# Kernel tuning notes

Hardware: AMD Instinct MI355X
Metric: run time of the kernel (lower is better)

## Reference

```python
import jax, jax.numpy as jnp
import numpy as np
import math

N_H = 16
REL_K = 16  # relative-position clamp window


def setup_inputs() -> dict:
    key = jax.random.key(0)
    ks = jax.random.split(key, 7)
    B, S, D = 8, 1024, 1024
    d_k = D // N_H
    scale = 0.02
    return {
        "x": jax.random.normal(ks[0], (B, S, D), dtype=jnp.float32),
        "W_attn": jax.random.normal(ks[1], (D, 3 * D), dtype=jnp.float32) * scale,
        "b_attn": jax.random.normal(ks[2], (3 * D,), dtype=jnp.float32) * scale,
        "W_proj": jax.random.normal(ks[3], (D, D), dtype=jnp.float32) * scale,
        "b_proj": jax.random.normal(ks[4], (D,), dtype=jnp.float32) * scale,
        "lut_k": jax.random.normal(ks[5], (2 * REL_K + 1, d_k), dtype=jnp.float32) * scale,
        "lut_v": jax.random.normal(ks[6], (2 * REL_K + 1, d_k), dtype=jnp.float32) * scale,
    }


def reference(x, W_attn, b_attn, W_proj, b_proj, lut_k, lut_v):
    B, S, D = x.shape
    d_k = D // N_H

    qkv = x @ W_attn + b_attn  # [B, S, 3D]
    q, k, v = jnp.split(qkv, 3, axis=-1)
    # [B, H, S, d_k]
    q = q.reshape(B, S, N_H, d_k).transpose(0, 2, 1, 3)
    k = k.reshape(B, S, N_H, d_k).transpose(0, 2, 1, 3)
    v = v.reshape(B, S, N_H, d_k).transpose(0, 2, 1, 3)

    i = jnp.arange(S)[:, None]
    j = jnp.arange(S)[None, :]
    rel = jnp.clip(j - i, -REL_K, REL_K) + REL_K  # [S, S] in [0, 2k]
    aij_k = lut_k[rel]  # [S, S, d_k]
    aij_v = lut_v[rel]  # [S, S, d_k]

    scores = jnp.einsum('bhid,bhjd->bhij', q, k)
    scores = scores + jnp.einsum('bhid,ijd->bhij', q, aij_k)
    scores = scores * (1.0 / math.sqrt(d_k))

    causal = j <= i  # [S, S]
    scores = jnp.where(causal[None, None, :, :], scores, -jnp.inf)
    attn = jax.nn.softmax(scores, axis=-1)  # [B, H, S, S]

    out = jnp.einsum('bhij,bhjd->bhid', attn, v)
    out = out + jnp.einsum('bhij,ijd->bhid', attn, aij_v)
    out = out.transpose(0, 2, 1, 3).reshape(B, S, D)
    return out @ W_proj + b_proj
```

## Files before the change

kernel.cpp:

```cpp
#include <hip/hip_runtime.h>
#include <hip/hip_bf16.h>
#include <math.h>

#define NH 16
#define S_LEN 1024
#define DK 64
#define D_MODEL 1024
#define HSZ 8388608

typedef __attribute__((ext_vector_type(8))) short bf16x8;
typedef __attribute__((ext_vector_type(4))) float f32x4;
typedef unsigned short USH;

#define EXPSCALE 0.1803368801111204f

__device__ __forceinline__ float fast_exp2(float x) {
    return __builtin_amdgcn_exp2f(x);
}

__device__ __forceinline__ short f2b(float x) {
    union { __hip_bfloat16 h; short s; } u;
    u.h = __float2bfloat16(x);
    return u.s;
}
__device__ __forceinline__ float b2f(USH u) {
    union { unsigned i; float f; } x;
    x.i = (unsigned)u << 16;
    return x.f;
}

__device__ __forceinline__ void gload16(const void* src, void* lds) {
    __builtin_amdgcn_global_load_lds(
        (const __attribute__((address_space(1))) void*)src,
        (__attribute__((address_space(3))) void*)lds,
        16, 0, 0);
}

__global__ __launch_bounds__(256)
void conv_bf16_kernel(const float* __restrict__ in, USH* __restrict__ out) {
    const int i = (blockIdx.x * 256 + threadIdx.x) * 8;
    const float4 a = *(const float4*)&in[i];
    const float4 b = *(const float4*)&in[i + 4];
    ushort4 o0, o1;
    o0.x = (USH)f2b(a.x); o0.y = (USH)f2b(a.y); o0.z = (USH)f2b(a.z); o0.w = (USH)f2b(a.w);
    o1.x = (USH)f2b(b.x); o1.y = (USH)f2b(b.y); o1.z = (USH)f2b(b.z); o1.w = (USH)f2b(b.w);
    *(ushort4*)&out[i] = o0;
    *(ushort4*)&out[i + 4] = o1;
}

__global__ __launch_bounds__(256)
void transp_bf16_kernel(const float* __restrict__ in, USH* __restrict__ out,
                        int R, int C) {
    __shared__ USH Ts[64][65];
    const int r0 = blockIdx.y * 64, c0 = blockIdx.x * 64;
    const int tr = threadIdx.x >> 4;
    const int tc4 = (threadIdx.x & 15) * 4;
    #pragma unroll
    for (int ph = 0; ph < 4; ++ph) {
        const int r = ph * 16 + tr;
        const float4 v = *(const float4*)&in[(size_t)(r0 + r) * C + c0 + tc4];
        Ts[tc4 + 0][r] = (USH)f2b(v.x);
        Ts[tc4 + 1][r] = (USH)f2b(v.y);
        Ts[tc4 + 2][r] = (USH)f2b(v.z);
        Ts[tc4 + 3][r] = (USH)f2b(v.w);
    }
    __syncthreads();
    #pragma unroll
    for (int ph = 0; ph < 4; ++ph) {
        const int cc = ph * 16 + tr;
        ushort4 o;
        o.x = Ts[cc][tc4 + 0]; o.y = Ts[cc][tc4 + 1];
        o.z = Ts[cc][tc4 + 2]; o.w = Ts[cc][tc4 + 3];
        *(ushort4*)&out[(size_t)(c0 + cc) * R + r0 + tc4] = o;
    }
}

__global__ __launch_bounds__(256)
void vtransp_kernel(const USH* __restrict__ in, USH* __restrict__ out) {
    __shared__ USH T[64][72];
    const int bh = blockIdx.x >> 4;
    const int s0 = (blockIdx.x & 15) * 64;
    const int r = threadIdx.x >> 4;
    const int c4 = (threadIdx.x & 15) * 4;
    #pragma unroll
    for (int ph = 0; ph < 4; ++ph) {
        const int row = ph * 16 + r;
        const ushort4 v = *(const ushort4*)
            &in[((size_t)bh * S_LEN + s0 + row) * DK + c4];
        T[row][c4 + 0] = v.x; T[row][c4 + 1] = v.y;
        T[row][c4 + 2] = v.z; T[row][c4 + 3] = v.w;
    }
    __syncthreads();
    #pragma unroll
    for (int ph = 0; ph < 4; ++ph) {
        const int d = ph * 16 + r;
        ushort4 o;
        o.x = T[c4 + 0][d]; o.y = T[c4 + 1][d];
        o.z = T[c4 + 2][d]; o.w = T[c4 + 3][d];
        *(ushort4*)&out[(size_t)bh * (S_LEN * DK) + (size_t)d * S_LEN + s0 + c4] = o;
    }
}

template<int QKV>
__global__ __launch_bounds__(256)
void mfma_gemm_kernel(const USH* __restrict__ A, const USH* __restrict__ Bt,
                      const float* __restrict__ bias,
                      float* __restrict__ Cf, USH* __restrict__ Cq,
                      USH* __restrict__ Ck, USH* __restrict__ Cv,
                      int M, int N, int K) {
    __shared__ __align__(16) USH As[128 * 32];
    __shared__ __align__(16) USH Bs[128 * 32];
    const int t = threadIdx.x;
    const int w = t >> 6, lane = t & 63, g = lane >> 4, c = lane & 15;
    const int wm = w >> 1, wn = w & 1;
    const int bm0 = blockIdx.y * 128, bn0 = blockIdx.x * 128;

    const int sk = ((t & 3) ^ ((t >> 3) & 3)) * 8;
    const USH* pa0 = A + (size_t)(bm0 + (t >> 2)) * K + sk;
    const USH* pa1 = pa0 + (size_t)64 * K;
    const USH* pb0 = Bt + (size_t)(bn0 + (t >> 2)) * K + sk;
    const USH* pb1 = pb0 + (size_t)64 * K;
    USH* ldsA0 = &As[(t & ~63) * 8];
    USH* ldsA1 = ldsA0 + 2048;
    USH* ldsB0 = &Bs[(t & ~63) * 8];
    USH* ldsB1 = ldsB0 + 2048;

    unsigned aoff[4], boff[4];
    #pragma unroll
    for (int i = 0; i < 4; ++i) {
        const int r = wm * 64 + i * 16 + c;
        aoff[i] = ((unsigned)(r * 64 + g * 16)) ^ ((((unsigned)r >> 1) & 3) << 4);
        const int n = wn * 64 + i * 16 + c;
        boff[i] = ((unsigned)(n * 64 + g * 16)) ^ ((((unsigned)n >> 1) & 3) << 4);
    }

    f32x4 acc[4][4];
    #pragma unroll
    for (int i = 0; i < 4; ++i)
        #pragma unroll
        for (int j = 0; j < 4; ++j) acc[i][j] = (f32x4)0.f;

    for (int k0 = 0; k0 < K; k0 += 32) {
        gload16(pa0 + k0, ldsA0);
        gload16(pa1 + k0, ldsA1);
        gload16(pb0 + k0, ldsB0);
        gload16(pb1 + k0, ldsB1);
        __syncthreads();

        bf16x8 af[4], bfr[4];
        #pragma unroll
        for (int i = 0; i < 4; ++i) af[i] = *(const bf16x8*)((const char*)As + aoff[i]);
        #pragma unroll
        for (int j = 0; j < 4; ++j) bfr[j] = *(const bf16x8*)((const char*)Bs + boff[j]);
        #pragma unroll
        for (int i = 0; i < 4; ++i)
            #pragma unroll
            for (int j = 0; j < 4; ++j)
                acc[i][j] = __builtin_amdgcn_mfma_f32_16x16x32_bf16(
                    af[i], bfr[j], acc[i][j], 0, 0, 0);
        __syncthreads();
    }

    #pragma unroll
    for (int i = 0; i < 4; ++i) {
        #pragma unroll
        for (int reg = 0; reg < 4; ++reg) {
            const int m = bm0 + wm * 64 + i * 16 + g * 4 + reg;
            #pragma unroll
            for (int j = 0; j < 4; ++j) {
                const int n = bn0 + wn * 64 + j * 16 + c;
                const float v = acc[i][j][reg] + bias[n];
                if (QKV) {
                    const int which = n >> 10;
                    const int h = (n & 1023) >> 6, d = n & 63;
                    const int b = m >> 10, s = m & 1023;
                    const size_t idx = (((size_t)(b * NH + h)) * S_LEN + s) * DK + d;
                    if (which == 0)      Cq[idx] = (USH)f2b(v);
                    else if (which == 1) Ck[idx] = (USH)f2b(v);
                    else                 Cv[idx] = (USH)f2b(v);
                } else {
                    Cf[(size_t)m * N + n] = v;
                }
            }
        }
    }
}

__global__ __launch_bounds__(512, 4)
void attn_mfma_kernel(const USH* __restrict__ qb,
                      const USH* __restrict__ kbuf,
                      const USH* __restrict__ vtg,
                      const float* __restrict__ lut_k,
                      const float* __restrict__ lut_v,
                      USH* __restrict__ ao) {
    const int bid = blockIdx.x;
    const int logical = (bid & 7) * 128 + (bid >> 3);
    const int ib = 7 - (logical & 7);
    const int bh = logical >> 3;
    const int b = bh >> 4, h = bh & 15;
    const int i0 = ib * 128;
    const int t = threadIdx.x;
    const int w = t >> 6;
    const int lane = t & 63;
    const int g = lane >> 4;
    const int c = lane & 15;

    __shared__ __align__(16) char smem[76928];
    char* pb     = smem + 49152;
    char* qsb    = smem + 49152;
    char* lutkb  = smem + 8192;
    USH* qrelb   = (USH*)(smem + 65536);
    USH* lvfb    = (USH*)(smem + 70656);
    USH* tapssb  = (USH*)(smem + 72832);

    const USH* qp  = qb   + (size_t)bh * (S_LEN * DK);
    const USH* kp  = kbuf + (size_t)bh * (S_LEN * DK);
    const USH* vtp = vtg  + (size_t)bh * (S_LEN * DK);

    auto stage = [&](int j0, int slot) {
        const int o = t * 16;
        const int row = o >> 7;
        const int chunk = (o >> 4) & 7;
        const int sc = (chunk ^ (row & 7)) * 8;
        gload16(kp + (size_t)(j0 + row) * DK + sc, smem + slot * 8192 + o);
        gload16(vtp + (size_t)row * S_LEN + j0 + sc, smem + 24576 + slot * 8192 + o);
    };

    stage(0, 0);
    for (int f = t; f < 2048; f += 512) {
        const int row = f >> 4, c4 = (f & 15) * 4;
        unsigned byte = ((unsigned)(row * 128 + c4 * 2)) ^ (((unsigned)row & 7) << 4);
        *(ushort4*)(qsb + byte) = *(const ushort4*)&qp[(size_t)(i0 + row) * DK + c4];
    }
    for (int e = t; e < 32 * 64; e += 512) {
        const int row = e >> 6, d = e & 63;
        const USH v = (row < 17) ? (USH)f2b(lut_k[row * 64 + d]) : (USH)0;
        unsigned byte = ((unsigned)(row * 128 + d * 2)) ^ (((unsigned)row & 7) << 4);
        *(USH*)(lutkb + byte) = v;
    }
    for (int e = t; e < 17 * 64; e += 512)
        lvfb[e] = (USH)f2b(lut_v[e]);
    __syncthreads();

    bf16x8 qa[2];
    {
        const int row = w * 16 + c;
        #pragma unroll
        for (int kh = 0; kh < 2; ++kh) {
            unsigned byte = ((unsigned)(row * 128 + kh * 64 + g * 16))
                          ^ (((unsigned)row & 7) << 4);
            qa[kh] = *(const bf16x8*)(qsb + byte);
        }
    }

    {
        f32x4 qr[2];
        qr[0] = (f32x4)0.f; qr[1] = (f32x4)0.f;
        #pragma unroll
        for (int sub2 = 0; sub2 < 2; ++sub2) {
            const int tap = sub2 * 16 + c;
            #pragma unroll
            for (int kh = 0; kh < 2; ++kh) {
                unsigned byte = ((unsigned)(tap * 128 + kh * 64 + g * 16))
                              ^ (((unsigned)tap & 7) << 4);
                bf16x8 lb = *(const bf16x8*)(lutkb + byte);
                qr[sub2] = __builtin_amdgcn_mfma_f32_16x16x32_bf16(
                    qa[kh], lb, qr[sub2], 0, 0, 0);
            }
        }
        #pragma unroll
        for (int sub2 = 0; sub2 < 2; ++sub2) {
            const int tap = sub2 * 16 + c;
            if (tap < 17) {
                #pragma unroll
                for (int r = 0; r < 4; ++r)
                    qrelb[(w * 16 + g * 4 + r) * 20 + tap] = (USH)f2b(qr[sub2][r]);
            }
        }
    }
    float qrel0s[4];
    #pragma unroll
    for (int r = 0; r < 4; ++r)
        qrel0s[r] = b2f(qrelb[(w * 16 + g * 4 + r) * 20]) * EXPSCALE;

    __syncthreads();

    const int NT = 2 * ib + 2;
    if (1 < NT) stage(64, 1);

    f32x4 acc[4];
    #pragma unroll
    for (int dt = 0; dt < 4; ++dt) acc[dt] = (f32x4)0.f;
    float l_r[4];
    #pragma unroll
    for (int r = 0; r < 4; ++r) l_r[r] = 0.f;

    const int wrow0 = i0 + w * 16;
    int cur = 0;
    for (int tile = 0; tile < NT; ++tile) {
        const int nxt2 = tile + 2;
        const int slot2 = (cur + 2 >= 3) ? cur - 1 : cur + 2;
        if (nxt2 < NT)
            stage(nxt2 << 6, slot2);

        if (tile * 64 > wrow0 + 15) {
            if (nxt2 < NT) asm volatile("s_waitcnt vmcnt(2)" ::: "memory");
            else           asm volatile("s_waitcnt vmcnt(0)" ::: "memory");
            __builtin_amdgcn_s_barrier();
            cur = (cur + 1 == 3) ? 0 : cur + 1;
            continue;
        }

        const char* ktb = smem + cur * 8192;
        const char* vtb = smem + 24576 + cur * 8192;

        float p[4][4];
        __builtin_amdgcn_s_setprio(1);
        f32x4 s[4];
        #pragma unroll
        for (int sub = 0; sub < 4; ++sub) {
            s[sub] = (f32x4)0.f;
            const int krow = sub * 16 + c;
            #pragma unroll
            for (int kh = 0; kh < 2; ++kh) {
                unsigned byte = ((unsigned)krow << 7) + ((unsigned)kh << 6) + ((unsigned)g << 4);
                byte ^= (unsigned)(krow & 7) << 4;
                bf16x8 kb = *(const bf16x8*)(ktb + byte);
                s[sub] = __builtin_amdgcn_mfma_f32_16x16x32_bf16(qa[kh], kb, s[sub], 0, 0, 0);
            }
        }
        __builtin_amdgcn_s_setprio(0);

        if (tile * 64 + 79 <= wrow0) {
            #pragma unroll
            for (int sub = 0; sub < 4; ++sub)
                #pragma unroll
                for (int r = 0; r < 4; ++r)
                    p[sub][r] = fast_exp2(s[sub][r] * EXPSCALE + qrel0s[r]);
        } else {
            #pragma unroll
            for (int sub = 0; sub < 4; ++sub) {
                const int dbase = tile * 64 + (sub * 16 + c) - i0 - (w * 16 + g * 4);
                #pragma unroll
                for (int r = 0; r < 4; ++r) {
                    const int dj = dbase - r;
                    int t17 = dj + 16;
                    t17 = t17 < 0 ? 0 : (t17 > 16 ? 16 : t17);
                    const int il = w * 16 + g * 4 + r;
                    float pv = fast_exp2((s[sub][r] + b2f(qrelb[il * 20 + t17])) * EXPSCALE);
                    if (dj > 0) pv = 0.f;
                    p[sub][r] = pv;
                    if (dj >= -15 && dj <= 0)
                        tapssb[il * 16 + dj + 15] = (USH)f2b(pv);
                }
            }
        }

        #pragma unroll
        for (int r = 0; r < 4; ++r)
            l_r[r] += (p[0][r] + p[1][r]) + (p[2][r] + p[3][r]);

        char* pw = pb + w * 2048;
        #pragma unroll
        for (int sub = 0; sub < 4; ++sub)
            #pragma unroll
            for (int r = 0; r < 4; ++r) {
                const int row = g * 4 + r;
                unsigned byte = ((unsigned)row << 7) + (((unsigned)(sub * 16 + c)) << 1);
                byte ^= (unsigned)(row & 7) << 4;
                *(short*)(pw + byte) = f2b(p[sub][r]);
            }

        bf16x8 pa[2];
        #pragma unroll
        for (int jh = 0; jh < 2; ++jh) {
            unsigned byte = ((unsigned)c << 7) + ((unsigned)jh << 6) + ((unsigned)g << 4);
            byte ^= (unsigned)(c & 7) << 4;
            pa[jh] = *(const bf16x8*)(pw + byte);
        }
        __builtin_amdgcn_s_setprio(1);
        #pragma unroll
        for (int dt = 0; dt < 4; ++dt) {
            const int d = dt * 16 + c;
            #pragma unroll
            for (int jh = 0; jh < 2; ++jh) {
                unsigned byte = ((unsigned)d << 7) + ((unsigned)jh << 6) + ((unsigned)g << 4);
                byte ^= (unsigned)(d & 7) << 4;
                bf16x8 vb = *(const bf16x8*)(vtb + byte);
                acc[dt] = __builtin_amdgcn_mfma_f32_16x16x32_bf16(pa[jh], vb, acc[dt], 0, 0, 0);
            }
        }
        __builtin_amdgcn_s_setprio(0);

        if (nxt2 < NT) asm volatile("s_waitcnt vmcnt(2)" ::: "memory");
        else           asm volatile("s_waitcnt vmcnt(0)" ::: "memory");
        __builtin_amdgcn_s_barrier();
        cur = (cur + 1 == 3) ? 0 : cur + 1;
    }

    const int rbase = w * 16 + g * 4;
    #pragma unroll
    for (int r = 0; r < 4; ++r) {
        float lsum = l_r[r];
        #pragma unroll
        for (int msk = 1; msk < 16; msk <<= 1)
            lsum += __shfl_xor(lsum, msk);
        const int il = rbase + r;
        float c0 = lsum;
        float tp[16];
        #pragma unroll
        for (int tap = 0; tap < 16; ++tap) {
            const int jg = i0 + il + tap - 15;
            const float pv = (jg >= 0) ? b2f(tapssb[il * 16 + tap]) : 0.f;
            tp[tap] = pv;
            c0 -= pv;
        }
        const float invl = 1.f / lsum;
        #pragma unroll
        for (int dt = 0; dt < 4; ++dt) {
            const int d = dt * 16 + c;
            float o = acc[dt][r] + c0 * b2f(lvfb[d]);
            #pragma unroll
            for (int tap = 0; tap < 16; ++tap)
                o += tp[tap] * b2f(lvfb[(tap + 1) * 64 + d]);
            o *= invl;
            ao[((size_t)b * S_LEN + (i0 + il)) * D_MODEL + h * DK + d] = (USH)f2b(o);
        }
    }
}

extern "C" void kernel_launch(void* const* d_in, const int* in_sizes, int n_in,
                              void* d_out, int out_size, void* d_ws, size_t ws_size,
                              hipStream_t stream) {
    const float* x      = (const float*)d_in[0];
    const float* W_attn = (const float*)d_in[1];
    const float* b_attn = (const float*)d_in[2];
    const float* W_proj = (const float*)d_in[3];
    const float* b_proj = (const float*)d_in[4];
    const float* lut_k  = (const float*)d_in[5];
    const float* lut_v  = (const float*)d_in[6];
    float* out = (float*)d_out;

    USH* qb    = (USH*)d_ws;
    USH* kb    = qb + HSZ;
    USH* vb    = kb + HSZ;
    USH* vtg   = vb + HSZ;
    USH* aob   = vtg + HSZ;
    USH* xb    = aob + HSZ;
    USH* watt  = xb + HSZ;
    USH* wproj = watt + 3145728;

    conv_bf16_kernel<<<HSZ / (256 * 8), 256, 0, stream>>>(x, xb);
    transp_bf16_kernel<<<dim3(3072 / 64, 1024 / 64), 256, 0, stream>>>(
        W_attn, watt, 1024, 3072);
    transp_bf16_kernel<<<dim3(1024 / 64, 1024 / 64), 256, 0, stream>>>(
        W_proj, wproj, 1024, 1024);

    mfma_gemm_kernel<1><<<dim3(3072 / 128, 8192 / 128), 256, 0, stream>>>(
        xb, watt, b_attn, nullptr, qb, kb, vb, 8192, 3072, 1024);

    vtransp_kernel<<<2048, 256, 0, stream>>>(vb, vtg);

    attn_mfma_kernel<<<1024, 512, 0, stream>>>(qb, kb, vtg, lut_k, lut_v, aob);

    mfma_gemm_kernel<0><<<dim3(1024 / 128, 8192 / 128), 256, 0, stream>>>(
        aob, wproj, b_proj, out, nullptr, nullptr, nullptr, 8192, 1024, 1024);
}
```

Baseline: 208.0 us.

## Merge prep kernels and rewrite QKV GEMM with 256x256 tiles and triple-buffered LDS

Merges the x conversion and both weight transposes into one prep kernel to save launches. Replaces the QKV GEMM with a 512-thread kernel using 256x256 output tiles and a three-slot LDS ring filled by direct global-to-LDS loads with vmcnt waits, plus s_setprio around the MFMAs and a swizzled block order for L2 reuse. This aims to increase data reuse per LDS byte and overlap global loads with MFMA work. It uses 96KB of LDS and a large accumulator set, which may limit occupancy.

Measured after the change: 199.2 us. -4.2%, faster.

```diff
diff --git a/kernel.cpp b/kernel.cpp
--- a/kernel.cpp
+++ b/kernel.cpp
@@ -37,24 +37,37 @@
 }
 
 __global__ __launch_bounds__(256)
-void conv_bf16_kernel(const float* __restrict__ in, USH* __restrict__ out) {
-    const int i = (blockIdx.x * 256 + threadIdx.x) * 8;
-    const float4 a = *(const float4*)&in[i];
-    const float4 b = *(const float4*)&in[i + 4];
-    ushort4 o0, o1;
-    o0.x = (USH)f2b(a.x); o0.y = (USH)f2b(a.y); o0.z = (USH)f2b(a.z); o0.w = (USH)f2b(a.w);
-    o1.x = (USH)f2b(b.x); o1.y = (USH)f2b(b.y); o1.z = (USH)f2b(b.z); o1.w = (USH)f2b(b.w);
-    *(ushort4*)&out[i] = o0;
-    *(ushort4*)&out[i + 4] = o1;
-}
-
-__global__ __launch_bounds__(256)
-void transp_bf16_kernel(const float* __restrict__ in, USH* __restrict__ out,
-                        int R, int C) {
+void prep_kernel(const float* __restrict__ x, USH* __restrict__ xb,
+                 const float* __restrict__ W_attn, USH* __restrict__ watt,
+                 const float* __restrict__ W_proj, USH* __restrict__ wproj) {
+    const int blk = blockIdx.x;
+    const int t = threadIdx.x;
+    if (blk < 4096) {
+        const int i = (blk * 256 + t) * 8;
+        const float4 a = *(const float4*)&x[i];
+        const float4 b = *(const float4*)&x[i + 4];
+        ushort4 o0, o1;
+        o0.x = (USH)f2b(a.x); o0.y = (USH)f2b(a.y); o0.z = (USH)f2b(a.z); o0.w = (USH)f2b(a.w);
+        o1.x = (USH)f2b(b.x); o1.y = (USH)f2b(b.y); o1.z = (USH)f2b(b.z); o1.w = (USH)f2b(b.w);
+        *(ushort4*)&xb[i] = o0;
+        *(ushort4*)&xb[i + 4] = o1;
+        return;
+    }
     __shared__ USH Ts[64][65];
-    const int r0 = blockIdx.y * 64, c0 = blockIdx.x * 64;
-    const int tr = threadIdx.x >> 4;
-    const int tc4 = (threadIdx.x & 15) * 4;
+    const float* in;
+    USH* out;
+    int R, C, r0, c0;
+    if (blk < 4864) {
+        const int idx = blk - 4096;
+        in = W_attn; out = watt; R = 1024; C = 3072;
+        c0 = (idx % 48) * 64; r0 = (idx / 48) * 64;
+    } else {
+        const int idx = blk - 4864;
+        in = W_proj; out = wproj; R = 1024; C = 1024;
+        c0 = (idx % 16) * 64; r0 = (idx / 16) * 64;
+    }
+    const int tr = t >> 4;
+    const int tc4 = (t & 15) * 4;
     #pragma unroll
     for (int ph = 0; ph < 4; ++ph) {
         const int r = ph * 16 + tr;
@@ -101,12 +114,109 @@
     }
 }
 
-template<int QKV>
+__global__ __launch_bounds__(512)
+void qkv_gemm_kernel(const USH* __restrict__ A, const USH* __restrict__ Bt,
+                     const float* __restrict__ bias,
+                     USH* __restrict__ Cq, USH* __restrict__ Ck,
+                     USH* __restrict__ Cv) {
+    __shared__ __align__(16) USH lds[3 * 16384];
+    const int t = threadIdx.x;
+    const int w = t >> 6, lane = t & 63, g = lane >> 4, c = lane & 15;
+    const int wm = w >> 2, wn = w & 3;
+    const int bid = blockIdx.x;
+    const int swz = (bid & 7) * 48 + (bid >> 3);
+    const int bn0 = (swz % 12) * 256;
+    const int bm0 = (swz / 12) * 256;
+
+    auto stage = [&](int kt, int slot) {
+        const int k0 = kt * 32;
+        USH* base = lds + slot * 16384;
+        #pragma unroll
+        for (int q = 0; q < 2; ++q) {
+            const int o = t * 16 + q * 8192;
+            const int row = o >> 6;
+            const int chunk = (o >> 4) & 3;
+            const int sc = (chunk ^ (row & 3)) * 8;
+            gload16(A + (size_t)(bm0 + row) * 1024 + k0 + sc, (char*)base + o);
+            gload16(Bt + (size_t)(bn0 + row) * 1024 + k0 + sc,
+                    (char*)(base + 8192) + o);
+        }
+    };
+
+    unsigned aoff[8], boff[4];
+    #pragma unroll
+    for (int i = 0; i < 8; ++i) {
+        const int row = wm * 128 + i * 16 + c;
+        aoff[i] = (unsigned)(row * 64) + (((unsigned)(g ^ (row & 3))) << 4);
+    }
+    #pragma unroll
+    for (int j = 0; j < 4; ++j) {
+        const int row = wn * 64 + j * 16 + c;
+        boff[j] = 16384u + (unsigned)(row * 64) + (((unsigned)(g ^ (row & 3))) << 4);
+    }
+
+    f32x4 acc[8][4];
+    #pragma unroll
+    for (int i = 0; i < 8; ++i)
+        #pragma unroll
+        for (int j = 0; j < 4; ++j) acc[i][j] = (f32x4)0.f;
+
+    stage(0, 0);
+    stage(1, 1);
+
+    int cur = 0;
+    for (int kt = 0; kt < 32; ++kt) {
+        if (kt < 31) asm volatile("s_waitcnt vmcnt(4)" ::: "memory");
+        else         asm volatile("s_waitcnt vmcnt(0)" ::: "memory");
+        __builtin_amdgcn_s_barrier();
+
+        const int slot2 = (cur + 2 >= 3) ? cur - 1 : cur + 2;
+        if (kt + 2 < 32)
+            stage(kt + 2, slot2);
+
+        const char* sb = (const char*)lds + cur * 32768;
+        bf16x8 af[8], bfr[4];
+        #pragma unroll
+        for (int i = 0; i < 8; ++i) af[i] = *(const bf16x8*)(sb + aoff[i]);
+        #pragma unroll
+        for (int j = 0; j < 4; ++j) bfr[j] = *(const bf16x8*)(sb + boff[j]);
+
+        __builtin_amdgcn_s_setprio(1);
+        #pragma unroll
+        for (int i = 0; i < 8; ++i)
+            #pragma unroll
+            for (int j = 0; j < 4; ++j)
+                acc[i][j] = __builtin_amdgcn_mfma_f32_16x16x32_bf16(
+                    af[i], bfr[j], acc[i][j], 0, 0, 0);
+        __builtin_amdgcn_s_setprio(0);
+
+        cur = (cur + 1 == 3) ? 0 : cur + 1;
+    }
+
+    #pragma unroll
+    for (int i = 0; i < 8; ++i) {
+        #pragma unroll
+        for (int reg = 0; reg < 4; ++reg) {
+            const int m = bm0 + wm * 128 + i * 16 + g * 4 + reg;
+            const int b = m >> 10, s = m & 1023;
+            #pragma unroll
+            for (int j = 0; j < 4; ++j) {
+                const int n = bn0 + wn * 64 + j * 16 + c;
+                const float v = acc[i][j][reg] + bias[n];
+                const int which = n >> 10;
+                const int h = (n & 1023) >> 6, d = n & 63;
+                const size_t idx = (((size_t)(b * NH + h)) * S_LEN + s) * DK + d;
+                if (which == 0)      Cq[idx] = (USH)f2b(v);
+                else if (which == 1) Ck[idx] = (USH)f2b(v);
+                else                 Cv[idx] = (USH)f2b(v);
+            }
+        }
+    }
+}
+
 __global__ __launch_bounds__(256)
-void mfma_gemm_kernel(const USH* __restrict__ A, const USH* __restrict__ Bt,
-                      const float* __restrict__ bias,
-                      float* __restrict__ Cf, USH* __restrict__ Cq,
-                      USH* __restrict__ Ck, USH* __restrict__ Cv,
+void proj_gemm_kernel(const USH* __restrict__ A, const USH* __restrict__ Bt,
+                      const float* __restrict__ bias, float* __restrict__ Cf,
                       int M, int N, int K) {
     __shared__ __align__(16) USH As[128 * 32];
     __shared__ __align__(16) USH Bs[128 * 32];
@@ -169,18 +279,7 @@
             #pragma unroll
             for (int j = 0; j < 4; ++j) {
                 const int n = bn0 + wn * 64 + j * 16 + c;
-                const float v = acc[i][j][reg] + bias[n];
-                if (QKV) {
-                    const int which = n >> 10;
-                    const int h = (n & 1023) >> 6, d = n & 63;
-                    const int b = m >> 10, s = m & 1023;
-                    const size_t idx = (((size_t)(b * NH + h)) * S_LEN + s) * DK + d;
-                    if (which == 0)      Cq[idx] = (USH)f2b(v);
-                    else if (which == 1) Ck[idx] = (USH)f2b(v);
-                    else                 Cv[idx] = (USH)f2b(v);
-                } else {
-                    Cf[(size_t)m * N + n] = v;
-                }
+                Cf[(size_t)m * N + n] = acc[i][j][reg] + bias[n];
             }
         }
     }
@@ -450,19 +549,14 @@
     USH* watt  = xb + HSZ;
     USH* wproj = watt + 3145728;
 
-    conv_bf16_kernel<<<HSZ / (256 * 8), 256, 0, stream>>>(x, xb);
-    transp_bf16_kernel<<<dim3(3072 / 64, 1024 / 64), 256, 0, stream>>>(
-        W_attn, watt, 1024, 3072);
-    transp_bf16_kernel<<<dim3(1024 / 64, 1024 / 64), 256, 0, stream>>>(
-        W_proj, wproj, 1024, 1024);
-
-    mfma_gemm_kernel<1><<<dim3(3072 / 128, 8192 / 128), 256, 0, stream>>>(
-        xb, watt, b_attn, nullptr, qb, kb, vb, 8192, 3072, 1024);
+    prep_kernel<<<5120, 256, 0, stream>>>(x, xb, W_attn, watt, W_proj, wproj);
+
+    qkv_gemm_kernel<<<384, 512, 0, stream>>>(xb, watt, b_attn, qb, kb, vb);
 
     vtransp_kernel<<<2048, 256, 0, stream>>>(vb, vtg);
 
     attn_mfma_kernel<<<1024, 512, 0, stream>>>(qb, kb, vtg, lut_k, lut_v, aob);
 
-    mfma_gemm_kernel<0><<<dim3(1024 / 128, 8192 / 128), 256, 0, stream>>>(
-        aob, wproj, b_proj, out, nullptr, nullptr, nullptr, 8192, 1024, 1024);
-}
+    proj_gemm_kernel<<<dim3(1024 / 128, 8192 / 128), 256, 0, stream>>>(
+        aob, wproj, b_proj, out, 8192, 1024, 1024);
+}
```
